# Optimization experiments

Hardware: AMD Instinct MI355X
Metric: run time of the kernel (lower is better)

The kernel has to match this reference:

```python
import jax, jax.numpy as jnp
import numpy as np

N = 6144      # number of pedestrians
HID = 256     # hidden_dim
OUT = 32      # out_dim
NTOP = 4      # n nearest neighbours
EMB = OUT // NTOP  # per-neighbour embedding dim = 8


def setup_inputs() -> dict:
    key = jax.random.key(0)
    ks = jax.random.split(key, 12)
    r = lambda k, shp, s=1.0: (jax.random.normal(k, shp, dtype=jnp.float32) * s)
    return {
        "obs1": r(ks[0], (N, 2)),
        "obs2": r(ks[1], (N, 2)),
        "h": r(ks[2], (N, HID), 0.1),
        "c": r(ks[3], (N, HID), 0.1),
        "W_emb": r(ks[4], (4, EMB), 0.3),
        "b_emb": r(ks[5], (EMB,), 0.1),
        "W_ih": r(ks[6], (4 * HID, OUT), 0.1),
        "b_ih": r(ks[7], (4 * HID,), 0.1),
        "W_hh": r(ks[8], (4 * HID, HID), 0.1),
        "b_hh": r(ks[9], (4 * HID,), 0.1),
        "W_pool": r(ks[10], (OUT, HID), 0.1),
        "b_pool": r(ks[11], (OUT,), 0.1),
    }


def reference(obs1, obs2, h, c, W_emb, b_emb, W_ih, b_ih, W_hh, b_hh, W_pool, b_pool):
    n = obs2.shape[0]
    vel = obs2 - obs1                                   # [N,2]
    # rel_position[i, j] = obs2[j] - obs2[i]
    diff = obs2[None, :, :] - obs2[:, None, :]          # [N,N,2]
    dist = jnp.linalg.norm(diff, axis=-1)               # [N,N]
    # exclude self (torch code drops the diagonal before topk)
    dist = jnp.where(jnp.eye(n, dtype=bool), jnp.inf, dist)
    _, idx = jax.lax.top_k(-dist, NTOP)                 # [N,NTOP] indices of nearest
    nearest_pos = jnp.take_along_axis(diff, idx[:, :, None], axis=1)  # [N,NTOP,2]
    # rel_direction[i, j] = vel[j] - vel[i]
    nearest_vel = vel[idx] - vel[:, None, :]            # [N,NTOP,2]
    feat = jnp.concatenate([nearest_pos, nearest_vel], axis=-1)       # [N,NTOP,4]
    # Linear(4, EMB) + ReLU, then flatten neighbours -> [N, OUT]
    emb = jax.nn.relu(feat @ W_emb + b_emb).reshape(n, -1)
    # LSTMCell (PyTorch gate order: i, f, g, o)
    gates = emb @ W_ih.T + b_ih + h @ W_hh.T + b_hh     # [N,4*HID]
    gi, gf, gg, go = jnp.split(gates, 4, axis=-1)
    c_new = jax.nn.sigmoid(gf) * c + jax.nn.sigmoid(gi) * jnp.tanh(gg)
    h_new = jax.nn.sigmoid(go) * jnp.tanh(c_new)
    out = h_new @ W_pool.T + b_pool                     # [N,OUT]
    return out
```

## Files before the change

### kernel.cpp

```cpp
#include <hip/hip_runtime.h>
#include <math.h>

typedef unsigned short u16;
typedef unsigned long long u64;
typedef __attribute__((ext_vector_type(8))) short bf16x8;
typedef __attribute__((ext_vector_type(4))) float f32x4;

__device__ __forceinline__ float sigf(float x)  { return 1.0f / (1.0f + __expf(-x)); }
__device__ __forceinline__ float tanhf_(float x){ float e = __expf(2.0f * x); return 1.0f - 2.0f / (e + 1.0f); }
__device__ __forceinline__ u16 f2bf(float f) {
    unsigned x = __float_as_uint(f);
    return (u16)((x + 0x7fffu + ((x >> 16) & 1u)) >> 16);
}

#define INSU(KEY) do {                                                              \
    u64 _k = (KEY);                                                                 \
    k3 = (_k < k3) ? _k : k3;                                                       \
    { bool _c = k3 < k2; u64 _lo = _c ? k3 : k2, _hi = _c ? k2 : k3; k2 = _lo; k3 = _hi; } \
    { bool _c = k2 < k1; u64 _lo = _c ? k2 : k1, _hi = _c ? k1 : k2; k1 = _lo; k2 = _hi; } \
    { bool _c = k1 < k0; u64 _lo = _c ? k1 : k0, _hi = _c ? k0 : k1; k0 = _lo; k1 = _hi; } \
} while (0)

#define INS4(D, J) do {                                                              \
    float _d = (D); int _j = (J);                                                    \
    if (_d < bd3 || (_d == bd3 && _j < bj3)) {                                       \
        bd3 = _d; bj3 = _j;                                                          \
        if (bd3 < bd2 || (bd3 == bd2 && bj3 < bj2)) {                                \
            float _t = bd2; bd2 = bd3; bd3 = _t; int _u = bj2; bj2 = bj3; bj3 = _u; }\
        if (bd2 < bd1 || (bd2 == bd1 && bj2 < bj1)) {                                \
            float _t = bd1; bd1 = bd2; bd2 = _t; int _u = bj1; bj1 = bj2; bj2 = _u; }\
        if (bd1 < bd0 || (bd1 == bd0 && bj1 < bj0)) {                                \
            float _t = bd0; bd0 = bd1; bd1 = _t; int _u = bj0; bj0 = bj1; bj1 = _u; }\
    } } while (0)

__global__ void diag_kernel(float* out, int code, int out_size) {
    if (out_size > 0) out[0] = (float)code * 1.0e8f;
}

__global__ __launch_bounds__(256) void knn_prep_kernel(
    const float* __restrict__ obs1, const float* __restrict__ obs2,
    const float* __restrict__ Wemb, const float* __restrict__ bemb,
    const float* __restrict__ Wih,  const float* __restrict__ Whh,
    const float* __restrict__ Wp,
    u16* __restrict__ Wgf, u16* __restrict__ Wpf,
    int n, int knn_blocks, float* __restrict__ out)
{
    const int t = threadIdx.x;

    if (blockIdx.x >= knn_blocks) {
        int id = (blockIdx.x - knn_blocks) * 256 + t;
        if (id < 36864) {
            int gt = id / 576, rem = id - gt * 576;
            int kt = rem >> 6, ln = rem & 63;
            int g  = gt * 16 + (ln & 15);
            int k  = kt * 32 + (ln >> 4) * 8;
            u16* dst = Wgf + (size_t)id * 8;
            #pragma unroll
            for (int j = 0; j < 8; j++) {
                int kk = k + j;
                float v = (kk < 32) ? Wih[(size_t)g * 32 + kk]
                                    : Whh[(size_t)g * 256 + (kk - 32)];
                dst[j] = f2bf(v);
            }
        } else if (id < 37888) {
            int id2 = id - 36864;
            int pt = id2 >> 9, rem = id2 & 511;
            int kt = rem >> 6, ln = rem & 63;
            int o  = pt * 16 + (ln & 15);
            int k  = kt * 32 + (ln >> 4) * 8;
            u16* dst = Wpf + (size_t)id2 * 8;
            #pragma unroll
            for (int j = 0; j < 8; j++)
                dst[j] = f2bf(Wp[(size_t)o * 256 + k + j]);
        }
        return;
    }

    const int lane = t & 63;
    const int wv   = t >> 6;
    const int i    = blockIdx.x * 4 + wv;
    if (i >= n) return;

    const float2* o2 = (const float2*)obs2;
    const float2 pi = o2[i];

    u64 k0 = ~0ull, k1 = ~0ull, k2 = ~0ull, k3 = ~0ull;

    int j = lane;
    for (; j + 192 < n; j += 256) {
        float2 p0 = o2[j], p1 = o2[j + 64], p2 = o2[j + 128], p3 = o2[j + 192];
        float dx, dy, d2, dd; u64 key;
        dx = p0.x - pi.x; dy = p0.y - pi.y;
        d2 = __fadd_rn(__fmul_rn(dx, dx), __fmul_rn(dy, dy));
        dd = __fsqrt_rn(d2);
        key = (((u64)__float_as_uint(dd)) << 24) | (unsigned)j;
        key = (j == i) ? ~0ull : key;                         INSU(key);
        dx = p1.x - pi.x; dy = p1.y - pi.y;
        d2 = __fadd_rn(__fmul_rn(dx, dx), __fmul_rn(dy, dy));
        dd = __fsqrt_rn(d2);
        key = (((u64)__float_as_uint(dd)) << 24) | (unsigned)(j + 64);
        key = (j + 64 == i) ? ~0ull : key;                    INSU(key);
        dx = p2.x - pi.x; dy = p2.y - pi.y;
        d2 = __fadd_rn(__fmul_rn(dx, dx), __fmul_rn(dy, dy));
        dd = __fsqrt_rn(d2);
        key = (((u64)__float_as_uint(dd)) << 24) | (unsigned)(j + 128);
        key = (j + 128 == i) ? ~0ull : key;                   INSU(key);
        dx = p3.x - pi.x; dy = p3.y - pi.y;
        d2 = __fadd_rn(__fmul_rn(dx, dx), __fmul_rn(dy, dy));
        dd = __fsqrt_rn(d2);
        key = (((u64)__float_as_uint(dd)) << 24) | (unsigned)(j + 192);
        key = (j + 192 == i) ? ~0ull : key;                   INSU(key);
    }
    for (; j < n; j += 64) {
        float2 pj = o2[j];
        float dx = pj.x - pi.x, dy = pj.y - pi.y;
        float d2 = __fadd_rn(__fmul_rn(dx, dx), __fmul_rn(dy, dy));
        float dd = __fsqrt_rn(d2);
        u64 key = (((u64)__float_as_uint(dd)) << 24) | (unsigned)j;
        key = (j == i) ? ~0ull : key;
        INSU(key);
    }

    #pragma unroll
    for (int m = 1; m < 64; m <<= 1) {
        u64 o0 = __shfl_xor(k0, m), o1 = __shfl_xor(k1, m);
        u64 o2_ = __shfl_xor(k2, m), o3 = __shfl_xor(k3, m);
        INSU(o0); INSU(o1); INSU(o2_); INSU(o3);
    }

    if (lane < 4) {
        u64 kq = (lane == 0) ? k0 : (lane == 1) ? k1 : (lane == 2) ? k2 : k3;
        int jn = (int)(kq & 0xFFFFFF);
        if (jn < 0 || jn >= n) jn = 0;
        float pix = pi.x, piy = pi.y;
        float pjx = obs2[2 * jn], pjy = obs2[2 * jn + 1];
        float px = pjx - pix, py = pjy - piy;
        float vix = pix - obs1[2 * i];
        float viy = piy - obs1[2 * i + 1];
        float vx = (pjx - obs1[2 * jn])     - vix;
        float vy = (pjy - obs1[2 * jn + 1]) - viy;
        float* dst = out + (size_t)i * 32 + lane * 8;
        #pragma unroll
        for (int e = 0; e < 8; e++) {
            float a = px * Wemb[e]      + py * Wemb[8 + e]
                    + vx * Wemb[16 + e] + vy * Wemb[24 + e]
                    + bemb[e];
            dst[e] = fmaxf(a, 0.0f);
        }
    }
}

__global__ __launch_bounds__(512) void lstm_kernel(
    const float* __restrict__ h,   const float* __restrict__ c,
    const u16*  __restrict__ Wgf,  const float* __restrict__ bih,
    const float* __restrict__ bhh,
    const u16*  __restrict__ Wpf,  const float* __restrict__ bp,
    int n, float* __restrict__ out)
{
    __shared__ __align__(16) char lds[17920];
    u16* sXb = (u16*)lds;
    u16* sHb = (u16*)(lds + 9472);

    const int t    = threadIdx.x;
    const int i0   = blockIdx.x * 16;
    const int lane = t & 63;
    const int wv   = t >> 6;
    const int fm   = lane & 15;
    const int fq   = lane >> 4;

    {
        int r = t >> 5, e = t & 31;
        int row = i0 + r;
        float v = (row < n) ? out[(size_t)row * 32 + e] : 0.0f;
        sXb[r * 296 + e] = f2bf(v);
    }
    #pragma unroll
    for (int f = t; f < 16 * 64; f += 512) {
        int r = f >> 6, k4 = f & 63;
        int row = i0 + r;
        float4 hv = (row < n) ? ((const float4*)h)[(size_t)row * 64 + k4]
                              : make_float4(0.f, 0.f, 0.f, 0.f);
        u16* d = &sXb[r * 296 + 32 + k4 * 4];
        d[0] = f2bf(hv.x); d[1] = f2bf(hv.y); d[2] = f2bf(hv.z); d[3] = f2bf(hv.w);
    }
    __syncthreads();

    bf16x8 afr[9];
    #pragma unroll
    for (int kt = 0; kt < 9; kt++)
        afr[kt] = *(const bf16x8*)&sXb[fm * 296 + kt * 32 + fq * 8];

    #pragma unroll
    for (int ut2 = 0; ut2 < 2; ut2++) {
        const int ut = wv * 2 + ut2;
        const int u  = ut * 16 + fm;

        f32x4 acc[4];
        #pragma unroll
        for (int jg = 0; jg < 4; jg++) acc[jg] = (f32x4){0.f, 0.f, 0.f, 0.f};

        #pragma unroll
        for (int jg = 0; jg < 4; jg++) {
            const int gt = jg * 16 + ut;
            const u16* wbase = Wgf + ((size_t)gt * 9) * 512 + lane * 8;
            #pragma unroll
            for (int kt = 0; kt < 9; kt++) {
                bf16x8 bfr = *(const bf16x8*)(wbase + kt * 512);
                acc[jg] = __builtin_amdgcn_mfma_f32_16x16x32_bf16(afr[kt], bfr, acc[jg], 0, 0, 0);
            }
        }

        float b0 = bih[u]       + bhh[u];
        float b1 = bih[u + 256] + bhh[u + 256];
        float b2 = bih[u + 512] + bhh[u + 512];
        float b3 = bih[u + 768] + bhh[u + 768];

        #pragma unroll
        for (int r_ = 0; r_ < 4; r_++) {
            int row = i0 + fq * 4 + r_;
            float cin = (row < n) ? c[(size_t)row * 256 + u] : 0.0f;
            float gi = acc[0][r_] + b0;
            float gf = acc[1][r_] + b1;
            float gg = acc[2][r_] + b2;
            float go = acc[3][r_] + b3;
            float cn = sigf(gf) * cin + sigf(gi) * tanhf_(gg);
            float hn = sigf(go) * tanhf_(cn);
            sHb[(fq * 4 + r_) * 264 + u] = f2bf(hn);
        }
    }
    __syncthreads();

    if (wv < 2) {
        bf16x8 ah[8];
        #pragma unroll
        for (int kt = 0; kt < 8; kt++)
            ah[kt] = *(const bf16x8*)&sHb[fm * 264 + kt * 32 + fq * 8];
        const u16* wbase = Wpf + ((size_t)wv * 8) * 512 + lane * 8;
        f32x4 acc = {0.f, 0.f, 0.f, 0.f};
        #pragma unroll
        for (int kt = 0; kt < 8; kt++) {
            bf16x8 bfr = *(const bf16x8*)(wbase + kt * 512);
            acc = __builtin_amdgcn_mfma_f32_16x16x32_bf16(ah[kt], bfr, acc, 0, 0, 0);
        }
        float bias = bp[wv * 16 + fm];
        #pragma unroll
        for (int r_ = 0; r_ < 4; r_++) {
            int row = i0 + fq * 4 + r_;
            if (row < n) out[(size_t)row * 32 + wv * 16 + fm] = acc[r_] + bias;
        }
    }
}

__global__ __launch_bounds__(256) void nnlstm_fallback(
    const float* __restrict__ obs1, const float* __restrict__ obs2,
    const float* __restrict__ h,    const float* __restrict__ c,
    const float* __restrict__ Wemb, const float* __restrict__ bemb,
    const float* __restrict__ Wih,  const float* __restrict__ bih,
    const float* __restrict__ Whh,  const float* __restrict__ bhh,
    const float* __restrict__ Wp,   const float* __restrict__ bp,
    int n, float* __restrict__ out)
{
    __shared__ float sMd[16][64];
    __shared__ int   sMj[16][64];
    __shared__ float sX[16][292];
    __shared__ float sH[16][264];

    const int t   = threadIdx.x;
    const int sub = t & 15;
    const int ii  = t >> 4;
    const int i0  = blockIdx.x * 16;
    const int i   = i0 + ii;

    for (int v = t; v < 16 * 256; v += 256) {
        int r = v >> 8, k = v & 255;
        int row = i0 + r;
        sX[r][32 + k] = (row < n) ? h[(size_t)row * 256 + k] : 0.0f;
    }

    float bd0 = 1e30f, bd1 = 1e30f, bd2 = 1e30f, bd3 = 1e30f;
    int   bj0 = 0x7fffffff, bj1 = 0x7fffffff, bj2 = 0x7fffffff, bj3 = 0x7fffffff;

    if (i < n) {
        const float pix = obs2[2 * i];
        const float piy = obs2[2 * i + 1];
        for (int j = sub; j < n; j += 16) {
            float dx = obs2[2 * j]     - pix;
            float dy = obs2[2 * j + 1] - piy;
            float d2 = __fadd_rn(__fmul_rn(dx, dx), __fmul_rn(dy, dy));
            float dist = __fsqrt_rn(d2);
            if (j == i) continue;
            INS4(dist, j);
        }
    }
    sMd[ii][sub * 4 + 0] = bd0;  sMj[ii][sub * 4 + 0] = bj0;
    sMd[ii][sub * 4 + 1] = bd1;  sMj[ii][sub * 4 + 1] = bj1;
    sMd[ii][sub * 4 + 2] = bd2;  sMj[ii][sub * 4 + 2] = bj2;
    sMd[ii][sub * 4 + 3] = bd3;  sMj[ii][sub * 4 + 3] = bj3;
    __syncthreads();

    if (t < 16) {
        const int r = t;
        const int irow = i0 + r;
        float bd0 = 1e30f, bd1 = 1e30f, bd2 = 1e30f, bd3 = 1e30f;
        int   bj0 = 0x7fffffff, bj1 = 0x7fffffff, bj2 = 0x7fffffff, bj3 = 0x7fffffff;
        for (int q = 0; q < 64; q++) { INS4(sMd[r][q], sMj[r][q]); }

        if (irow < n) {
            float pix = obs2[2 * irow], piy = obs2[2 * irow + 1];
            float vix = pix - obs1[2 * irow];
            float viy = piy - obs1[2 * irow + 1];
            #pragma unroll
            for (int q2 = 0; q2 < 4; q2++) {
                int jn = (q2 == 0) ? bj0 : (q2 == 1) ? bj1 : (q2 == 2) ? bj2 : bj3;
                if (jn < 0 || jn >= n) jn = 0;
                float pjx = obs2[2 * jn], pjy = obs2[2 * jn + 1];
                float px = pjx - pix, py = pjy - piy;
                float vx = (pjx - obs1[2 * jn])     - vix;
                float vy = (pjy - obs1[2 * jn + 1]) - viy;
                #pragma unroll
                for (int e = 0; e < 8; e++) {
                    float a = px * Wemb[e]      + py * Wemb[8 + e]
                            + vx * Wemb[16 + e] + vy * Wemb[24 + e]
                            + bemb[e];
                    sX[r][q2 * 8 + e] = fmaxf(a, 0.0f);
                }
            }
        } else {
            for (int e = 0; e < 32; e++) sX[r][e] = 0.0f;
        }
    }
    __syncthreads();

    const int uu = t;
    float acc[4][16];
    #pragma unroll
    for (int j = 0; j < 4; j++) {
        float b = bih[uu + 256 * j] + bhh[uu + 256 * j];
        #pragma unroll
        for (int r = 0; r < 16; r++) acc[j][r] = b;
    }

    for (int kc = 0; kc < 288; kc++) {
        float w[4];
        #pragma unroll
        for (int j = 0; j < 4; j++) {
            int g = uu + 256 * j;
            w[j] = (kc < 32) ? Wih[(size_t)g * 32 + kc]
                             : Whh[(size_t)g * 256 + (kc - 32)];
        }
        #pragma unroll
        for (int r = 0; r < 16; r++) {
            float x = sX[r][kc];
            #pragma unroll
            for (int j = 0; j < 4; j++) acc[j][r] += w[j] * x;
        }
    }

    for (int r = 0; r < 16; r++) {
        int row = i0 + r;
        float cin = (row < n) ? c[(size_t)row * 256 + uu] : 0.0f;
        float cn = sigf(acc[1][r]) * cin + sigf(acc[0][r]) * tanhf(acc[2][r]);
        float hn = sigf(acc[3][r]) * tanhf(cn);
        sH[r][uu] = hn;
    }
    __syncthreads();

    for (int v = t; v < 16 * 32; v += 256) {
        int r = v >> 5, o = v & 31;
        int row = i0 + r;
        if (row >= n) continue;
        float a = bp[o];
        for (int kc = 0; kc < 256; kc++)
            a += Wp[(size_t)o * 256 + kc] * sH[r][kc];
        out[(size_t)row * 32 + o] = a;
    }
}

extern "C" void kernel_launch(void* const* d_in, const int* in_sizes, int n_in,
                              void* d_out, int out_size, void* d_ws, size_t ws_size,
                              hipStream_t stream) {
    float* out = (float*)d_out;

    int code = 0, n = 0;
    if (n_in != 12) code = 1;
    else {
        n = in_sizes[1] / 2;
        if (n <= 4 || in_sizes[1] != 2 * n)          code = 2;
        else if (in_sizes[0]  != 2 * n)              code = 3;
        else if (in_sizes[2]  != 256 * n)            code = 4;
        else if (in_sizes[3]  != 256 * n)            code = 5;
        else if (in_sizes[4]  != 32 || in_sizes[5] != 8)        code = 6;
        else if (in_sizes[6]  != 32768 || in_sizes[7] != 1024)  code = 7;
        else if (in_sizes[8]  != 262144 || in_sizes[9] != 1024) code = 8;
        else if (in_sizes[10] != 8192 || in_sizes[11] != 32)    code = 9;
        else if (out_size != 32 * n)                 code = 10;
    }
    if (code != 0) {
        diag_kernel<<<1, 1, 0, stream>>>(out, code, out_size);
        return;
    }

    const float* obs1   = (const float*)d_in[0];
    const float* obs2   = (const float*)d_in[1];
    const float* h      = (const float*)d_in[2];
    const float* c      = (const float*)d_in[3];
    const float* W_emb  = (const float*)d_in[4];
    const float* b_emb  = (const float*)d_in[5];
    const float* W_ih   = (const float*)d_in[6];
    const float* b_ih   = (const float*)d_in[7];
    const float* W_hh   = (const float*)d_in[8];
    const float* b_hh   = (const float*)d_in[9];
    const float* W_pool = (const float*)d_in[10];
    const float* b_pool = (const float*)d_in[11];

    const size_t wgf_bytes = (size_t)36864 * 8 * sizeof(u16);
    const size_t wpf_bytes = (size_t)1024 * 8 * sizeof(u16);

    if (ws_size >= wgf_bytes + wpf_bytes && n <= (1 << 24)) {
        u16* Wgf = (u16*)d_ws;
        u16* Wpf = (u16*)((char*)d_ws + wgf_bytes);
        int knn_blocks = (n + 3) / 4;
        knn_prep_kernel<<<knn_blocks + 148, 256, 0, stream>>>(
            obs1, obs2, W_emb, b_emb, W_ih, W_hh, W_pool, Wgf, Wpf,
            n, knn_blocks, out);
        lstm_kernel<<<(n + 15) / 16, 512, 0, stream>>>(
            h, c, Wgf, b_ih, b_hh, Wpf, b_pool, n, out);
    } else {
        nnlstm_fallback<<<(n + 15) / 16, 256, 0, stream>>>(
            obs1, obs2, h, c, W_emb, b_emb, W_ih, b_ih, W_hh, b_hh,
            W_pool, b_pool, n, out);
    }
}
```

Measured before the change: 153.1 us.

## Fuse kNN search and embedding into the LSTM kernel via shared memory

```diff
diff --git a/kernel.cpp b/kernel.cpp
--- a/kernel.cpp
+++ b/kernel.cpp
@@ -37,124 +37,45 @@
     if (out_size > 0) out[0] = (float)code * 1.0e8f;
 }
 
-__global__ __launch_bounds__(256) void knn_prep_kernel(
+__global__ __launch_bounds__(256) void prep_kernel(
+    const float* __restrict__ Wih, const float* __restrict__ Whh,
+    const float* __restrict__ Wp,
+    u16* __restrict__ Wgf, u16* __restrict__ Wpf)
+{
+    int id = blockIdx.x * 256 + threadIdx.x;
+    if (id < 36864) {
+        int gt = id / 576, rem = id - gt * 576;
+        int kt = rem >> 6, ln = rem & 63;
+        int g  = gt * 16 + (ln & 15);
+        int k  = kt * 32 + (ln >> 4) * 8;
+        u16* dst = Wgf + (size_t)id * 8;
+        #pragma unroll
+        for (int j = 0; j < 8; j++) {
+            int kk = k + j;
+            float v = (kk < 32) ? Wih[(size_t)g * 32 + kk]
+                                : Whh[(size_t)g * 256 + (kk - 32)];
+            dst[j] = f2bf(v);
+        }
+    } else if (id < 37888) {
+        int id2 = id - 36864;
+        int pt = id2 >> 9, rem = id2 & 511;
+        int kt = rem >> 6, ln = rem & 63;
+        int o  = pt * 16 + (ln & 15);
+        int k  = kt * 32 + (ln >> 4) * 8;
+        u16* dst = Wpf + (size_t)id2 * 8;
+        #pragma unroll
+        for (int j = 0; j < 8; j++)
+            dst[j] = f2bf(Wp[(size_t)o * 256 + k + j]);
+    }
+}
+
+__global__ __launch_bounds__(512) void fused_kernel(
     const float* __restrict__ obs1, const float* __restrict__ obs2,
+    const float* __restrict__ h,    const float* __restrict__ c,
     const float* __restrict__ Wemb, const float* __restrict__ bemb,
-    const float* __restrict__ Wih,  const float* __restrict__ Whh,
-    const float* __restrict__ Wp,
-    u16* __restrict__ Wgf, u16* __restrict__ Wpf,
-    int n, int knn_blocks, float* __restrict__ out)
-{
-    const int t = threadIdx.x;
-
-    if (blockIdx.x >= knn_blocks) {
-        int id = (blockIdx.x - knn_blocks) * 256 + t;
-        if (id < 36864) {
-            int gt = id / 576, rem = id - gt * 576;
-            int kt = rem >> 6, ln = rem & 63;
-            int g  = gt * 16 + (ln & 15);
-            int k  = kt * 32 + (ln >> 4) * 8;
-            u16* dst = Wgf + (size_t)id * 8;
-            #pragma unroll
-            for (int j = 0; j < 8; j++) {
-                int kk = k + j;
-                float v = (kk < 32) ? Wih[(size_t)g * 32 + kk]
-                                    : Whh[(size_t)g * 256 + (kk - 32)];
-                dst[j] = f2bf(v);
-            }
-        } else if (id < 37888) {
-            int id2 = id - 36864;
-            int pt = id2 >> 9, rem = id2 & 511;
-            int kt = rem >> 6, ln = rem & 63;
-            int o  = pt * 16 + (ln & 15);
-            int k  = kt * 32 + (ln >> 4) * 8;
-            u16* dst = Wpf + (size_t)id2 * 8;
-            #pragma unroll
-            for (int j = 0; j < 8; j++)
-                dst[j] = f2bf(Wp[(size_t)o * 256 + k + j]);
-        }
-        return;
-    }
-
-    const int lane = t & 63;
-    const int wv   = t >> 6;
-    const int i    = blockIdx.x * 4 + wv;
-    if (i >= n) return;
-
-    const float2* o2 = (const float2*)obs2;
-    const float2 pi = o2[i];
-
-    u64 k0 = ~0ull, k1 = ~0ull, k2 = ~0ull, k3 = ~0ull;
-
-    int j = lane;
-    for (; j + 192 < n; j += 256) {
-        float2 p0 = o2[j], p1 = o2[j + 64], p2 = o2[j + 128], p3 = o2[j + 192];
-        float dx, dy, d2, dd; u64 key;
-        dx = p0.x - pi.x; dy = p0.y - pi.y;
-        d2 = __fadd_rn(__fmul_rn(dx, dx), __fmul_rn(dy, dy));
-        dd = __fsqrt_rn(d2);
-        key = (((u64)__float_as_uint(dd)) << 24) | (unsigned)j;
-        key = (j == i) ? ~0ull : key;                         INSU(key);
-        dx = p1.x - pi.x; dy = p1.y - pi.y;
-        d2 = __fadd_rn(__fmul_rn(dx, dx), __fmul_rn(dy, dy));
-        dd = __fsqrt_rn(d2);
-        key = (((u64)__float_as_uint(dd)) << 24) | (unsigned)(j + 64);
-        key = (j + 64 == i) ? ~0ull : key;                    INSU(key);
-        dx = p2.x - pi.x; dy = p2.y - pi.y;
-        d2 = __fadd_rn(__fmul_rn(dx, dx), __fmul_rn(dy, dy));
-        dd = __fsqrt_rn(d2);
-        key = (((u64)__float_as_uint(dd)) << 24) | (unsigned)(j + 128);
-        key = (j + 128 == i) ? ~0ull : key;                   INSU(key);
-        dx = p3.x - pi.x; dy = p3.y - pi.y;
-        d2 = __fadd_rn(__fmul_rn(dx, dx), __fmul_rn(dy, dy));
-        dd = __fsqrt_rn(d2);
-        key = (((u64)__float_as_uint(dd)) << 24) | (unsigned)(j + 192);
-        key = (j + 192 == i) ? ~0ull : key;                   INSU(key);
-    }
-    for (; j < n; j += 64) {
-        float2 pj = o2[j];
-        float dx = pj.x - pi.x, dy = pj.y - pi.y;
-        float d2 = __fadd_rn(__fmul_rn(dx, dx), __fmul_rn(dy, dy));
-        float dd = __fsqrt_rn(d2);
-        u64 key = (((u64)__float_as_uint(dd)) << 24) | (unsigned)j;
-        key = (j == i) ? ~0ull : key;
-        INSU(key);
-    }
-
-    #pragma unroll
-    for (int m = 1; m < 64; m <<= 1) {
-        u64 o0 = __shfl_xor(k0, m), o1 = __shfl_xor(k1, m);
-        u64 o2_ = __shfl_xor(k2, m), o3 = __shfl_xor(k3, m);
-        INSU(o0); INSU(o1); INSU(o2_); INSU(o3);
-    }
-
-    if (lane < 4) {
-        u64 kq = (lane == 0) ? k0 : (lane == 1) ? k1 : (lane == 2) ? k2 : k3;
-        int jn = (int)(kq & 0xFFFFFF);
-        if (jn < 0 || jn >= n) jn = 0;
-        float pix = pi.x, piy = pi.y;
-        float pjx = obs2[2 * jn], pjy = obs2[2 * jn + 1];
-        float px = pjx - pix, py = pjy - piy;
-        float vix = pix - obs1[2 * i];
-        float viy = piy - obs1[2 * i + 1];
-        float vx = (pjx - obs1[2 * jn])     - vix;
-        float vy = (pjy - obs1[2 * jn + 1]) - viy;
-        float* dst = out + (size_t)i * 32 + lane * 8;
-        #pragma unroll
-        for (int e = 0; e < 8; e++) {
-            float a = px * Wemb[e]      + py * Wemb[8 + e]
-                    + vx * Wemb[16 + e] + vy * Wemb[24 + e]
-                    + bemb[e];
-            dst[e] = fmaxf(a, 0.0f);
-        }
-    }
-}
-
-__global__ __launch_bounds__(512) void lstm_kernel(
-    const float* __restrict__ h,   const float* __restrict__ c,
-    const u16*  __restrict__ Wgf,  const float* __restrict__ bih,
+    const u16*  __restrict__ Wgf,   const float* __restrict__ bih,
     const float* __restrict__ bhh,
-    const u16*  __restrict__ Wpf,  const float* __restrict__ bp,
+    const u16*  __restrict__ Wpf,   const float* __restrict__ bp,
     int n, float* __restrict__ out)
 {
     __shared__ __align__(16) char lds[17920];
@@ -167,13 +88,9 @@
     const int wv   = t >> 6;
     const int fm   = lane & 15;
     const int fq   = lane >> 4;
-
-    {
-        int r = t >> 5, e = t & 31;
-        int row = i0 + r;
-        float v = (row < n) ? out[(size_t)row * 32 + e] : 0.0f;
-        sXb[r * 296 + e] = f2bf(v);
-    }
+    const int l32  = lane & 31;
+    const int half = lane >> 5;
+
     #pragma unroll
     for (int f = t; f < 16 * 64; f += 512) {
         int r = f >> 6, k4 = f & 63;
@@ -182,6 +99,85 @@
                               : make_float4(0.f, 0.f, 0.f, 0.f);
         u16* d = &sXb[r * 296 + 32 + k4 * 4];
         d[0] = f2bf(hv.x); d[1] = f2bf(hv.y); d[2] = f2bf(hv.z); d[3] = f2bf(hv.w);
+    }
+
+    const int pr = wv * 2 + half;
+    const int i  = i0 + pr;
+    const bool alive = (i < n);
+
+    const float2* o2 = (const float2*)obs2;
+    const float2 pi = alive ? o2[i] : make_float2(0.f, 0.f);
+
+    u64 k0 = ~0ull, k1 = ~0ull, k2 = ~0ull, k3 = ~0ull;
+
+    if (alive) {
+        int j = l32;
+        for (; j + 96 < n; j += 128) {
+            float2 p0 = o2[j], p1 = o2[j + 32], p2 = o2[j + 64], p3 = o2[j + 96];
+            float dx, dy, d2, dd; u64 key;
+            dx = p0.x - pi.x; dy = p0.y - pi.y;
+            d2 = __fadd_rn(__fmul_rn(dx, dx), __fmul_rn(dy, dy));
+            dd = __fsqrt_rn(d2);
+            key = (((u64)__float_as_uint(dd)) << 24) | (unsigned)j;
+            key = (j == i) ? ~0ull : key;                        INSU(key);
+            dx = p1.x - pi.x; dy = p1.y - pi.y;
+            d2 = __fadd_rn(__fmul_rn(dx, dx), __fmul_rn(dy, dy));
+            dd = __fsqrt_rn(d2);
+            key = (((u64)__float_as_uint(dd)) << 24) | (unsigned)(j + 32);
+            key = (j + 32 == i) ? ~0ull : key;                   INSU(key);
+            dx = p2.x - pi.x; dy = p2.y - pi.y;
+            d2 = __fadd_rn(__fmul_rn(dx, dx), __fmul_rn(dy, dy));
+            dd = __fsqrt_rn(d2);
+            key = (((u64)__float_as_uint(dd)) << 24) | (unsigned)(j + 64);
+            key = (j + 64 == i) ? ~0ull : key;                   INSU(key);
+            dx = p3.x - pi.x; dy = p3.y - pi.y;
+            d2 = __fadd_rn(__fmul_rn(dx, dx), __fmul_rn(dy, dy));
+            dd = __fsqrt_rn(d2);
+            key = (((u64)__float_as_uint(dd)) << 24) | (unsigned)(j + 96);
+            key = (j + 96 == i) ? ~0ull : key;                   INSU(key);
+        }
+        for (; j < n; j += 32) {
+            float2 pj = o2[j];
+            float dx = pj.x - pi.x, dy = pj.y - pi.y;
+            float d2 = __fadd_rn(__fmul_rn(dx, dx), __fmul_rn(dy, dy));
+            float dd = __fsqrt_rn(d2);
+            u64 key = (((u64)__float_as_uint(dd)) << 24) | (unsigned)j;
+            key = (j == i) ? ~0ull : key;
+            INSU(key);
+        }
+    }
+
+    #pragma unroll
+    for (int m = 1; m < 32; m <<= 1) {
+        u64 o0 = __shfl_xor(k0, m), o1 = __shfl_xor(k1, m);
+        u64 o2_ = __shfl_xor(k2, m), o3 = __shfl_xor(k3, m);
+        INSU(o0); INSU(o1); INSU(o2_); INSU(o3);
+    }
+
+    if (l32 < 4) {
+        if (alive) {
+            u64 kq = (l32 == 0) ? k0 : (l32 == 1) ? k1 : (l32 == 2) ? k2 : k3;
+            int jn = (int)(kq & 0xFFFFFF);
+            if (jn < 0 || jn >= n) jn = 0;
+            float pjx = obs2[2 * jn], pjy = obs2[2 * jn + 1];
+            float px = pjx - pi.x, py = pjy - pi.y;
+            float vix = pi.x - obs1[2 * i];
+            float viy = pi.y - obs1[2 * i + 1];
+            float vx = (pjx - obs1[2 * jn])     - vix;
+            float vy = (pjy - obs1[2 * jn + 1]) - viy;
+            u16* dst = &sXb[pr * 296 + l32 * 8];
+            #pragma unroll
+            for (int e = 0; e < 8; e++) {
+                float a = px * Wemb[e]      + py * Wemb[8 + e]
+                        + vx * Wemb[16 + e] + vy * Wemb[24 + e]
+                        + bemb[e];
+                dst[e] = f2bf(fmaxf(a, 0.0f));
+            }
+        } else {
+            u16* dst = &sXb[pr * 296 + l32 * 8];
+            #pragma unroll
+            for (int e = 0; e < 8; e++) dst[e] = 0;
+        }
     }
     __syncthreads();
 
@@ -419,12 +415,9 @@
     if (ws_size >= wgf_bytes + wpf_bytes && n <= (1 << 24)) {
         u16* Wgf = (u16*)d_ws;
         u16* Wpf = (u16*)((char*)d_ws + wgf_bytes);
-        int knn_blocks = (n + 3) / 4;
-        knn_prep_kernel<<<knn_blocks + 148, 256, 0, stream>>>(
-            obs1, obs2, W_emb, b_emb, W_ih, W_hh, W_pool, Wgf, Wpf,
-            n, knn_blocks, out);
-        lstm_kernel<<<(n + 15) / 16, 512, 0, stream>>>(
-            h, c, Wgf, b_ih, b_hh, Wpf, b_pool, n, out);
+        prep_kernel<<<148, 256, 0, stream>>>(W_ih, W_hh, W_pool, Wgf, Wpf);
+        fused_kernel<<<(n + 15) / 16, 512, 0, stream>>>(
+            obs1, obs2, h, c, W_emb, b_emb, Wgf, b_ih, b_hh, Wpf, b_pool, n, out);
     } else {
         nnlstm_fallback<<<(n + 15) / 16, 256, 0, stream>>>(
             obs1, obs2, h, c, W_emb, b_emb, W_ih, b_ih, W_hh, b_hh,
```

Measured after the change: 168.3 us. +9.9%, slower.
